# Performance work log

Hardware: AMD Instinct MI355X
Metric: run time of the kernel (lower is better)

## Reference

```python
import jax, jax.numpy as jnp
import numpy as np

QMAX8 = 127.0  # 2**(8-1)-1


def quant1(x, scale):
    # 1-bit symmetric quant: s * sign(x), s = |scale| (per-group mean scale)
    return jnp.abs(scale) * jnp.sign(x)


def quant8(x, scale):
    s = jnp.maximum(jnp.abs(scale), 1e-8)
    q = jnp.clip(jnp.round(x / s), -QMAX8, QMAX8)
    return q * s


def setup_inputs() -> dict:
    key = jax.random.key(0)
    ks = jax.random.split(key, 5)
    p, j, k, m, l, n = 2, 32, 32, 32, 8, 32
    x = jax.random.normal(ks[0], (2, 1024, k * n), dtype=jnp.float32)
    Y_fp = jax.random.normal(ks[1], (p, j, k, m, l), dtype=jnp.float32)
    Z_fp = jax.random.normal(ks[2], (p, j, k, l, n), dtype=jnp.float32)
    A = jax.random.normal(ks[3], (p, j, k, 4), dtype=jnp.float32)
    bias = jax.random.normal(ks[4], (j * m,), dtype=jnp.float32)
    act_scale = jnp.full((1,), 0.001, dtype=jnp.float32)
    return {"x": x, "Y_fp": Y_fp, "Z_fp": Z_fp, "A": A, "bias": bias,
            "act_scale": act_scale}


def reference(x, Y_fp, Z_fp, A, bias, act_scale):
    p, j, k, m, l = Y_fp.shape
    n = Z_fp.shape[-1]
    orig_shape = x.shape[:-1]
    X = x.astype(jnp.float32)
    X = quant8(X, act_scale)  # activation quantization (act_bits=8)

    # per-(p,j,k) mean-abs scales over last two dims
    Y_scale = jnp.mean(jnp.abs(Y_fp), axis=(-2, -1), keepdims=True)
    Z_scale = jnp.mean(jnp.abs(Z_fp), axis=(-2, -1), keepdims=True)
    Y_q = quant1(Y_fp, Y_scale)  # (p,j,k,m,l)
    Z_q = quant1(Z_fp, Z_scale)  # (p,j,k,l,n)

    X_kn = X.reshape(-1, k, n)  # (B,k,n)
    T = jnp.einsum('bkn,pjkln->bpjkl', X_kn, Z_q)
    core = jnp.einsum('pjkml,bpjkl->bpjkm', Y_q, T)

    # quant_bias=True correction terms
    a = A[..., 0][None, ..., None]            # (1,p,j,k,1)
    out1 = jnp.sum(core * a, axis=(1, 3))     # (B,j,m)
    Y_sum = jnp.sum(Y_q, axis=-1)             # (p,j,k,m)
    B_coef = jnp.sum(A[..., 1][..., None] * Y_sum, axis=0)  # (j,k,m)
    Sx = jnp.sum(X_kn, axis=-1)               # (B,k)
    out2 = jnp.einsum('bk,jkm->bjm', Sx, B_coef)
    Zs = jnp.sum(Z_q, axis=-2)                # (p,j,k,n)
    Tz = jnp.einsum('bkn,pjkn->bpjk', X_kn, Zs)
    out3 = jnp.sum(Tz * A[..., 2][None], axis=(1, 3))[..., None]  # (B,j,1)
    D_coef = jnp.sum(A[..., 3], axis=0)       # (j,k)
    out4 = jnp.einsum('bk,jk->bj', Sx, D_coef)[..., None]          # (B,j,1)

    out_bjm = out1 + out2 + out3 + out4       # (B,j,m) via broadcast
    out_2d = out_bjm.reshape(-1, j * m) + bias
    out = out_2d.reshape(*orig_shape, j * m)
    return out.astype(x.dtype)
```

## Files before the change

### kernel.cpp

```cpp
#include <hip/hip_runtime.h>
#include <math.h>
#include <stdint.h>


typedef __attribute__((ext_vector_type(8))) short bf16x8;
typedef __attribute__((ext_vector_type(4))) float f32x4;
typedef __attribute__((ext_vector_type(4))) unsigned short us4;

__device__ __forceinline__ float fsign(float v) {
    return (v > 0.f) ? 1.f : ((v < 0.f) ? -1.f : 0.f);
}

__device__ __forceinline__ unsigned short f2bf(float f) {
    union { float f; uint32_t u; } c; c.f = f;
    uint32_t r = 0x7fffu + ((c.u >> 16) & 1u);
    return (unsigned short)((c.u + r) >> 16);
}

__device__ __forceinline__ void gl2lds16(const void* g, void* l) {
    __builtin_amdgcn_global_load_lds(
        (const __attribute__((address_space(1))) void*)g,
        (__attribute__((address_space(3))) void*)l, 16, 0, 0);
}

__global__ __launch_bounds__(256) void fused_pre(
    const float* __restrict__ Y,
    const float* __restrict__ Z,
    const float* __restrict__ A,
    const float* __restrict__ x,
    const float* __restrict__ act_scale,
    unsigned short* __restrict__ wt,
    unsigned short* __restrict__ qx)
{
    const int t = threadIdx.x;

    if (blockIdx.x >= 1024) {
        const float s = fmaxf(fabsf(act_scale[0]), 1e-8f);
        const int b2 = blockIdx.x - 1024;
        #pragma unroll
        for (int it = 0; it < 4; ++it) {
            const size_t i4 = (size_t)b2 * 256 + t + (size_t)it * 131072;
            const float4 v = *(const float4*)(x + i4 * 4);
            us4 o;
            o.x = f2bf(fminf(fmaxf(rintf(v.x / s), -127.f), 127.f));
            o.y = f2bf(fminf(fmaxf(rintf(v.y / s), -127.f), 127.f));
            o.z = f2bf(fminf(fmaxf(rintf(v.z / s), -127.f), 127.f));
            o.w = f2bf(fminf(fmaxf(rintf(v.w / s), -127.f), 127.f));
            *(us4*)(qx + i4 * 4) = o;
        }
        return;
    }

    __shared__ float sgy[2][256];
    __shared__ float sgz[2][256];
    __shared__ float wred[16];

    const int jk = blockIdx.x;
    const int jj = jk >> 5;
    const int kk = jk & 31;
    const int n  = t & 31;
    const int mb = t >> 5;

    const int base0 = jj * 32 + kk;
    const int base1 = 1024 + base0;

    const float yv0 = Y[(size_t)base0 * 256 + t];
    const float yv1 = Y[(size_t)base1 * 256 + t];
    const float zv0 = Z[(size_t)base0 * 256 + t];
    const float zv1 = Z[(size_t)base1 * 256 + t];
    const float a00 = A[(size_t)base0 * 4 + 0], a01 = A[(size_t)base0 * 4 + 1];
    const float a02 = A[(size_t)base0 * 4 + 2], a03 = A[(size_t)base0 * 4 + 3];
    const float a10 = A[(size_t)base1 * 4 + 0], a11 = A[(size_t)base1 * 4 + 1];
    const float a12 = A[(size_t)base1 * 4 + 2], a13 = A[(size_t)base1 * 4 + 3];

    sgy[0][t] = fsign(yv0);
    sgy[1][t] = fsign(yv1);
    sgz[0][t] = fsign(zv0);
    sgz[1][t] = fsign(zv1);

    float ay0 = fabsf(yv0), az0 = fabsf(zv0);
    float ay1 = fabsf(yv1), az1 = fabsf(zv1);
    #pragma unroll
    for (int d = 1; d < 64; d <<= 1) {
        ay0 += __shfl_xor(ay0, d, 64);
        az0 += __shfl_xor(az0, d, 64);
        ay1 += __shfl_xor(ay1, d, 64);
        az1 += __shfl_xor(az1, d, 64);
    }
    if ((t & 63) == 0) {
        const int w = t >> 6;
        wred[w * 4 + 0] = ay0;
        wred[w * 4 + 1] = az0;
        wred[w * 4 + 2] = ay1;
        wred[w * 4 + 3] = az1;
    }
    __syncthreads();

    const float sY0 = (wred[0] + wred[4] + wred[8]  + wred[12]) * (1.f / 256.f);
    const float sZ0 = (wred[1] + wred[5] + wred[9]  + wred[13]) * (1.f / 256.f);
    const float sY1 = (wred[2] + wred[6] + wred[10] + wred[14]) * (1.f / 256.f);
    const float sZ1 = (wred[3] + wred[7] + wred[11] + wred[15]) * (1.f / 256.f);

    float zcol0 = 0.f, zcol1 = 0.f;
    #pragma unroll
    for (int l = 0; l < 8; ++l) {
        zcol0 += sgz[0][l * 32 + n];
        zcol1 += sgz[1][l * 32 + n];
    }

    #pragma unroll
    for (int q = 0; q < 4; ++q) {
        const int m = mb + 8 * q;
        float ysum0 = 0.f, w0 = 0.f, ysum1 = 0.f, w1 = 0.f;
        #pragma unroll
        for (int l = 0; l < 8; ++l) {
            const float ys0 = sgy[0][m * 8 + l];
            const float ys1 = sgy[1][m * 8 + l];
            ysum0 += ys0;
            ysum1 += ys1;
            w0 += ys0 * sgz[0][l * 32 + n];
            w1 += ys1 * sgz[1][l * 32 + n];
        }
        const float acc =
            a00 * sY0 * sZ0 * w0 + a01 * sY0 * ysum0 + a02 * sZ0 * zcol0 + a03 +
            a10 * sY1 * sZ1 * w1 + a11 * sY1 * ysum1 + a12 * sZ1 * zcol1 + a13;
        wt[(size_t)(jj * 32 + m) * 1024 + kk * 32 + n] = f2bf(acc);
    }
}

__global__ __launch_bounds__(256) void gemm_mfma(
    const unsigned short* __restrict__ qx,
    const unsigned short* __restrict__ wt,
    const float* __restrict__ bias,
    const float* __restrict__ act_scale,
    float* __restrict__ out)
{
    __shared__ __align__(16) short lds[3 * 6144];

    const int tid  = threadIdx.x;
    const int lane = tid & 63;
    const int wave = tid >> 6;
    const int wm = wave >> 1;
    const int wn = wave & 1;
    const int rowBase = blockIdx.y * 64;
    const int colBase = blockIdx.x * 128;

    const float s = fmaxf(fabsf(act_scale[0]), 1e-8f);

    f32x4 acc[2][4];
    #pragma unroll
    for (int i = 0; i < 2; ++i)
        #pragma unroll
        for (int jx = 0; jx < 4; ++jx)
            acc[i][jx] = (f32x4)0.f;

    const unsigned short* agp =
        qx + (size_t)(rowBase + (tid >> 2)) * 1024 + (tid & 3) * 8;
    const unsigned short* bgp0 =
        wt + (size_t)(colBase + (tid >> 2)) * 1024 + (tid & 3) * 8;
    const unsigned short* bgp1 = bgp0 + (size_t)64 * 1024;

    char* const ldsc = (char*)lds;
    const int q4  = lane >> 4;
    const int l16 = lane & 15;
    const int woff = wave * 1024;

    #pragma unroll
    for (int tpre = 0; tpre < 3; ++tpre) {
        char* b = ldsc + tpre * 12288;
        gl2lds16(agp  + tpre * 32, b + woff);
        gl2lds16(bgp0 + tpre * 32, b + 4096 + woff);
        gl2lds16(bgp1 + tpre * 32, b + 8192 + woff);
    }

    #pragma unroll 1
    for (int kt = 0; kt < 32; ++kt) {
        if (kt < 30)       asm volatile("s_waitcnt vmcnt(6)" ::: "memory");
        else if (kt == 30) asm volatile("s_waitcnt vmcnt(3)" ::: "memory");
        else               asm volatile("s_waitcnt vmcnt(0)" ::: "memory");
        __builtin_amdgcn_s_barrier();

        const int cur = kt % 3;
        const short* As = lds + cur * 6144;
        const short* Bs = As + 2048;

        bf16x8 af[2], bfr[4];
        #pragma unroll
        for (int im = 0; im < 2; ++im)
            af[im] = *(const bf16x8*)&As[(wm * 32 + im * 16 + l16) * 32 + q4 * 8];
        #pragma unroll
        for (int in = 0; in < 4; ++in)
            bfr[in] = *(const bf16x8*)&Bs[(wn * 64 + in * 16 + l16) * 32 + q4 * 8];

        asm volatile("s_waitcnt lgkmcnt(0)" ::: "memory");
        __builtin_amdgcn_s_barrier();

        if (kt + 3 < 32) {
            const int k3 = (kt + 3) * 32;
            char* b = ldsc + cur * 12288;
            gl2lds16(agp  + k3, b + woff);
            gl2lds16(bgp0 + k3, b + 4096 + woff);
            gl2lds16(bgp1 + k3, b + 8192 + woff);
        }

        #pragma unroll
        for (int im = 0; im < 2; ++im)
            #pragma unroll
            for (int in = 0; in < 4; ++in)
                acc[im][in] = __builtin_amdgcn_mfma_f32_16x16x32_bf16(
                    af[im], bfr[in], acc[im][in], 0, 0, 0);
    }

    #pragma unroll
    for (int im = 0; im < 2; ++im) {
        #pragma unroll
        for (int in = 0; in < 4; ++in) {
            const int col = colBase + wn * 64 + in * 16 + l16;
            const float b = bias[col];
            #pragma unroll
            for (int r = 0; r < 4; ++r) {
                const int row = rowBase + wm * 32 + im * 16 + q4 * 4 + r;
                out[(size_t)row * 1024 + col] = s * acc[im][in][r] + b;
            }
        }
    }
}

extern "C" void kernel_launch(void* const* d_in, const int* in_sizes, int n_in,
                              void* d_out, int out_size, void* d_ws, size_t ws_size,
                              hipStream_t stream) {
    const float* x         = (const float*)d_in[0];
    const float* Y_fp      = (const float*)d_in[1];
    const float* Z_fp      = (const float*)d_in[2];
    const float* A         = (const float*)d_in[3];
    const float* bias      = (const float*)d_in[4];
    const float* act_scale = (const float*)d_in[5];
    float* out = (float*)d_out;

    unsigned short* wt = (unsigned short*)d_ws;
    unsigned short* qx = (unsigned short*)((char*)d_ws + 2 * 1024 * 1024);

    fused_pre<<<dim3(1536), dim3(256), 0, stream>>>(Y_fp, Z_fp, A, x, act_scale, wt, qx);
    gemm_mfma<<<dim3(8, 32), dim3(256), 0, stream>>>(qx, wt, bias, act_scale, out);
}
```

Before: 86.95 us.

## Bit-pack sign weights with ballot/popcount and retile GEMM to 64x64 swizzled double buffer

The preprocessing kernel now stores the signs of Y and Z as ballot bitmasks in shared memory instead of float sign arrays. It computes the sign dot products and row and column sums with xor and popcount, which cuts LDS traffic and ALU work. The GEMM tile shrinks from 64x128 to 64x64 with a K step of 64 and a double-buffered LDS using an XOR swizzle to avoid bank conflicts. This doubles the grid to 512 blocks for better CU occupancy, at the cost of less operand reuse per block and a plain __syncthreads pipeline instead of explicit vmcnt waits. One side effect is that sign(0) is now treated as +1 rather than 0, which only differs for exact zeros.

```diff
diff --git a/kernel.cpp b/kernel.cpp
--- a/kernel.cpp
+++ b/kernel.cpp
@@ -6,10 +6,6 @@
 typedef __attribute__((ext_vector_type(8))) short bf16x8;
 typedef __attribute__((ext_vector_type(4))) float f32x4;
 typedef __attribute__((ext_vector_type(4))) unsigned short us4;
-
-__device__ __forceinline__ float fsign(float v) {
-    return (v > 0.f) ? 1.f : ((v < 0.f) ? -1.f : 0.f);
-}
 
 __device__ __forceinline__ unsigned short f2bf(float f) {
     union { float f; uint32_t u; } c; c.f = f;
@@ -51,8 +47,8 @@
         return;
     }
 
-    __shared__ float sgy[2][256];
-    __shared__ float sgz[2][256];
+    __shared__ unsigned int yb[2][8];
+    __shared__ unsigned int zb[2][8];
     __shared__ float wred[16];
 
     const int jk = blockIdx.x;
@@ -60,6 +56,8 @@
     const int kk = jk & 31;
     const int n  = t & 31;
     const int mb = t >> 5;
+    const int w  = t >> 6;
+    const int lane = t & 63;
 
     const int base0 = jj * 32 + kk;
     const int base1 = 1024 + base0;
@@ -73,10 +71,16 @@
     const float a10 = A[(size_t)base1 * 4 + 0], a11 = A[(size_t)base1 * 4 + 1];
     const float a12 = A[(size_t)base1 * 4 + 2], a13 = A[(size_t)base1 * 4 + 3];
 
-    sgy[0][t] = fsign(yv0);
-    sgy[1][t] = fsign(yv1);
-    sgz[0][t] = fsign(zv0);
-    sgz[1][t] = fsign(zv1);
+    const unsigned long long by0 = __ballot(yv0 < 0.f);
+    const unsigned long long by1 = __ballot(yv1 < 0.f);
+    const unsigned long long bz0 = __ballot(zv0 < 0.f);
+    const unsigned long long bz1 = __ballot(zv1 < 0.f);
+    if (lane == 0) {
+        yb[0][2 * w] = (unsigned)by0; yb[0][2 * w + 1] = (unsigned)(by0 >> 32);
+        yb[1][2 * w] = (unsigned)by1; yb[1][2 * w + 1] = (unsigned)(by1 >> 32);
+        zb[0][2 * w] = (unsigned)bz0; zb[0][2 * w + 1] = (unsigned)(bz0 >> 32);
+        zb[1][2 * w] = (unsigned)bz1; zb[1][2 * w + 1] = (unsigned)(bz1 >> 32);
+    }
 
     float ay0 = fabsf(yv0), az0 = fabsf(zv0);
     float ay1 = fabsf(yv1), az1 = fabsf(zv1);
@@ -87,8 +91,7 @@
         ay1 += __shfl_xor(ay1, d, 64);
         az1 += __shfl_xor(az1, d, 64);
     }
-    if ((t & 63) == 0) {
-        const int w = t >> 6;
+    if (lane == 0) {
         wred[w * 4 + 0] = ay0;
         wred[w * 4 + 1] = az0;
         wred[w * 4 + 2] = ay1;
@@ -101,29 +104,33 @@
     const float sY1 = (wred[2] + wred[6] + wred[10] + wred[14]) * (1.f / 256.f);
     const float sZ1 = (wred[3] + wred[7] + wred[11] + wred[15]) * (1.f / 256.f);
 
-    float zcol0 = 0.f, zcol1 = 0.f;
+    const float c00 = a00 * sY0 * sZ0, c01 = a01 * sY0, c02 = a02 * sZ0;
+    const float c10 = a10 * sY1 * sZ1, c11 = a11 * sY1, c12 = a12 * sZ1;
+    const float cb  = a03 + a13;
+
+    unsigned sz0 = 0, sz1 = 0;
     #pragma unroll
     for (int l = 0; l < 8; ++l) {
-        zcol0 += sgz[0][l * 32 + n];
-        zcol1 += sgz[1][l * 32 + n];
-    }
+        sz0 |= ((zb[0][l] >> n) & 1u) << l;
+        sz1 |= ((zb[1][l] >> n) & 1u) << l;
+    }
+    const float zc0 = 8.f - 2.f * (float)__popc(sz0);
+    const float zc1 = 8.f - 2.f * (float)__popc(sz1);
+    const float czc = c02 * zc0 + c12 * zc1 + cb;
+
+    const int ybw = (mb >> 2);
+    const int ybs = (mb & 3) * 8;
 
     #pragma unroll
     for (int q = 0; q < 4; ++q) {
         const int m = mb + 8 * q;
-        float ysum0 = 0.f, w0 = 0.f, ysum1 = 0.f, w1 = 0.f;
-        #pragma unroll
-        for (int l = 0; l < 8; ++l) {
-            const float ys0 = sgy[0][m * 8 + l];
-            const float ys1 = sgy[1][m * 8 + l];
-            ysum0 += ys0;
-            ysum1 += ys1;
-            w0 += ys0 * sgz[0][l * 32 + n];
-            w1 += ys1 * sgz[1][l * 32 + n];
-        }
-        const float acc =
-            a00 * sY0 * sZ0 * w0 + a01 * sY0 * ysum0 + a02 * sZ0 * zcol0 + a03 +
-            a10 * sY1 * sZ1 * w1 + a11 * sY1 * ysum1 + a12 * sZ1 * zcol1 + a13;
+        const unsigned sy0 = (yb[0][2 * q + ybw] >> ybs) & 0xffu;
+        const unsigned sy1 = (yb[1][2 * q + ybw] >> ybs) & 0xffu;
+        const float w0  = 8.f - 2.f * (float)__popc(sy0 ^ sz0);
+        const float w1  = 8.f - 2.f * (float)__popc(sy1 ^ sz1);
+        const float ys0 = 8.f - 2.f * (float)__popc(sy0);
+        const float ys1 = 8.f - 2.f * (float)__popc(sy1);
+        const float acc = c00 * w0 + c01 * ys0 + c10 * w1 + c11 * ys1 + czc;
         wt[(size_t)(jj * 32 + m) * 1024 + kk * 32 + n] = f2bf(acc);
     }
 }
@@ -135,7 +142,7 @@
     const float* __restrict__ act_scale,
     float* __restrict__ out)
 {
-    __shared__ __align__(16) short lds[3 * 6144];
+    __shared__ __align__(16) short lds[2 * 8192];
 
     const int tid  = threadIdx.x;
     const int lane = tid & 63;
@@ -143,79 +150,84 @@
     const int wm = wave >> 1;
     const int wn = wave & 1;
     const int rowBase = blockIdx.y * 64;
-    const int colBase = blockIdx.x * 128;
+    const int colBase = blockIdx.x * 64;
 
     const float s = fmaxf(fabsf(act_scale[0]), 1e-8f);
 
-    f32x4 acc[2][4];
+    f32x4 acc[2][2];
     #pragma unroll
     for (int i = 0; i < 2; ++i)
         #pragma unroll
-        for (int jx = 0; jx < 4; ++jx)
+        for (int jx = 0; jx < 2; ++jx)
             acc[i][jx] = (f32x4)0.f;
 
-    const unsigned short* agp =
-        qx + (size_t)(rowBase + (tid >> 2)) * 1024 + (tid & 3) * 8;
-    const unsigned short* bgp0 =
-        wt + (size_t)(colBase + (tid >> 2)) * 1024 + (tid & 3) * 8;
-    const unsigned short* bgp1 = bgp0 + (size_t)64 * 1024;
+    const int lr = lane >> 3;
+    const int kx = (lane & 7) ^ lr;
+    const unsigned short* ag[2];
+    const unsigned short* bg[2];
+    #pragma unroll
+    for (int i = 0; i < 2; ++i) {
+        const int g = i * 4 + wave;
+        ag[i] = qx + (size_t)(rowBase + g * 8 + lr) * 1024 + kx * 8;
+        bg[i] = wt + (size_t)(colBase + g * 8 + lr) * 1024 + kx * 8;
+    }
 
     char* const ldsc = (char*)lds;
     const int q4  = lane >> 4;
     const int l16 = lane & 15;
-    const int woff = wave * 1024;
-
-    #pragma unroll
-    for (int tpre = 0; tpre < 3; ++tpre) {
-        char* b = ldsc + tpre * 12288;
-        gl2lds16(agp  + tpre * 32, b + woff);
-        gl2lds16(bgp0 + tpre * 32, b + 4096 + woff);
-        gl2lds16(bgp1 + tpre * 32, b + 8192 + woff);
-    }
-
-    #pragma unroll 1
-    for (int kt = 0; kt < 32; ++kt) {
-        if (kt < 30)       asm volatile("s_waitcnt vmcnt(6)" ::: "memory");
-        else if (kt == 30) asm volatile("s_waitcnt vmcnt(3)" ::: "memory");
-        else               asm volatile("s_waitcnt vmcnt(0)" ::: "memory");
-        __builtin_amdgcn_s_barrier();
-
-        const int cur = kt % 3;
-        const short* As = lds + cur * 6144;
-        const short* Bs = As + 2048;
-
-        bf16x8 af[2], bfr[4];
-        #pragma unroll
-        for (int im = 0; im < 2; ++im)
-            af[im] = *(const bf16x8*)&As[(wm * 32 + im * 16 + l16) * 32 + q4 * 8];
-        #pragma unroll
-        for (int in = 0; in < 4; ++in)
-            bfr[in] = *(const bf16x8*)&Bs[(wn * 64 + in * 16 + l16) * 32 + q4 * 8];
-
-        asm volatile("s_waitcnt lgkmcnt(0)" ::: "memory");
-        __builtin_amdgcn_s_barrier();
-
-        if (kt + 3 < 32) {
-            const int k3 = (kt + 3) * 32;
-            char* b = ldsc + cur * 12288;
-            gl2lds16(agp  + k3, b + woff);
-            gl2lds16(bgp0 + k3, b + 4096 + woff);
-            gl2lds16(bgp1 + k3, b + 8192 + woff);
-        }
-
-        #pragma unroll
-        for (int im = 0; im < 2; ++im)
-            #pragma unroll
-            for (int in = 0; in < 4; ++in)
-                acc[im][in] = __builtin_amdgcn_mfma_f32_16x16x32_bf16(
-                    af[im], bfr[in], acc[im][in], 0, 0, 0);
+
+    #pragma unroll
+    for (int i = 0; i < 2; ++i) {
+        const int g = i * 4 + wave;
+        gl2lds16(ag[i], ldsc + g * 1024);
+        gl2lds16(bg[i], ldsc + 8192 + g * 1024);
+    }
+
+    for (int kt = 0; kt < 16; ++kt) {
+        __syncthreads();
+
+        if (kt + 1 < 16) {
+            const int k1 = (kt + 1) * 64;
+            char* bb = ldsc + ((kt + 1) & 1) * 16384;
+            #pragma unroll
+            for (int i = 0; i < 2; ++i) {
+                const int g = i * 4 + wave;
+                gl2lds16(ag[i] + k1, bb + g * 1024);
+                gl2lds16(bg[i] + k1, bb + 8192 + g * 1024);
+            }
+        }
+
+        const short* As = lds + (kt & 1) * 8192;
+        const short* Bs = As + 4096;
+
+        #pragma unroll
+        for (int kk2 = 0; kk2 < 2; ++kk2) {
+            const int kc = kk2 * 4 + q4;
+            bf16x8 af[2], bfr[2];
+            #pragma unroll
+            for (int im = 0; im < 2; ++im) {
+                const int r = wm * 32 + im * 16 + l16;
+                af[im] = *(const bf16x8*)&As[(r * 8 + (kc ^ (r & 7))) * 8];
+            }
+            #pragma unroll
+            for (int in = 0; in < 2; ++in) {
+                const int r = wn * 32 + in * 16 + l16;
+                bfr[in] = *(const bf16x8*)&Bs[(r * 8 + (kc ^ (r & 7))) * 8];
+            }
+            #pragma unroll
+            for (int im = 0; im < 2; ++im)
+                #pragma unroll
+                for (int in = 0; in < 2; ++in)
+                    acc[im][in] = __builtin_amdgcn_mfma_f32_16x16x32_bf16(
+                        af[im], bfr[in], acc[im][in], 0, 0, 0);
+        }
     }
 
     #pragma unroll
     for (int im = 0; im < 2; ++im) {
         #pragma unroll
-        for (int in = 0; in < 4; ++in) {
-            const int col = colBase + wn * 64 + in * 16 + l16;
+        for (int in = 0; in < 2; ++in) {
+            const int col = colBase + wn * 32 + in * 16 + l16;
             const float b = bias[col];
             #pragma unroll
             for (int r = 0; r < 4; ++r) {
@@ -237,9 +249,9 @@
     const float* act_scale = (const float*)d_in[5];
     float* out = (float*)d_out;
 
-    unsigned short* wt = (unsigned short*)d_ws;
-    unsigned short* qx = (unsigned short*)((char*)d_ws + 2 * 1024 * 1024);
-
-    fused_pre<<<dim3(1536), dim3(256), 0, stream>>>(Y_fp, Z_fp, A, x, act_scale, wt, qx);
-    gemm_mfma<<<dim3(8, 32), dim3(256), 0, stream>>>(qx, wt, bias, act_scale, out);
-}
+    unsigned short* wtp = (unsigned short*)d_ws;
+    unsigned short* qxp = (unsigned short*)((char*)d_ws + 2 * 1024 * 1024);
+
+    fused_pre<<<dim3(1536), dim3(256), 0, stream>>>(Y_fp, Z_fp, A, x, act_scale, wtp, qxp);
+    gemm_mfma<<<dim3(16, 32), dim3(256), 0, stream>>>(qxp, wtp, bias, act_scale, out);
+}
```

After: 82.69 us. 4.9% less time.
